# Performance work log

Hardware: AMD Instinct MI355X
Metric: run time of the kernel (lower is better)

The kernel has to match this reference:

```python
import jax, jax.numpy as jnp
import numpy as np

N_NODES = 10000
N_EDGES = 160000
IN_DIM = 512
HID = 256
HEADS = 4
OUT_DIM = 512
NEG_SLOPE = 0.2  # PyG GATConv default


def _glorot(key, shape):
    fan_in, fan_out = shape[0], shape[-1]
    lim = jnp.sqrt(6.0 / (fan_in + fan_out))
    return jax.random.uniform(key, shape, jnp.float32, -lim, lim)


def setup_inputs() -> dict:
    key = jax.random.key(0)
    ks = jax.random.split(key, 16)
    x = jax.random.normal(ks[0], (N_NODES, IN_DIM), jnp.float32)
    edge_index = jax.random.randint(ks[1], (2, N_EDGES), 0, N_NODES, jnp.int64)
    # layer 1: GATConv(512 -> 256, heads=4, concat) -> out 1024
    W1 = _glorot(ks[2], (IN_DIM, HEADS * HID))
    att_src1 = _glorot(ks[3], (HEADS, HID))
    att_dst1 = _glorot(ks[4], (HEADS, HID))
    b1 = jnp.zeros((HEADS * HID,), jnp.float32)
    # layer 2: GATConv(1024 -> 256, heads=4, concat) -> out 1024
    W2 = _glorot(ks[5], (HEADS * HID, HEADS * HID))
    att_src2 = _glorot(ks[6], (HEADS, HID))
    att_dst2 = _glorot(ks[7], (HEADS, HID))
    b2 = jnp.zeros((HEADS * HID,), jnp.float32)
    # final fc: 1024 -> 512
    fcW = _glorot(ks[8], (HEADS * HID, OUT_DIM))
    fcb = jnp.zeros((OUT_DIM,), jnp.float32)
    return dict(x=x, edge_index=edge_index, W1=W1, att_src1=att_src1,
                att_dst1=att_dst1, b1=b1, W2=W2, att_src2=att_src2,
                att_dst2=att_dst2, b2=b2, fcW=fcW, fcb=fcb)


def gat_conv(x, src, dst, W, att_src, att_dst, bias):
    # x: [N, F_in]; src/dst: [E] (self-loops already included)
    N = x.shape[0]
    h = (x @ W).reshape(N, HEADS, HID)                       # [N, H, C]
    a_src = jnp.sum(h * att_src, axis=-1)                    # [N, H]
    a_dst = jnp.sum(h * att_dst, axis=-1)                    # [N, H]
    e = jax.nn.leaky_relu(a_src[src] + a_dst[dst], NEG_SLOPE)  # [E, H]
    # numerically stable segment softmax over destination nodes
    m = jax.ops.segment_max(e, dst, num_segments=N)          # [N, H]
    e = jnp.exp(e - m[dst])
    s = jax.ops.segment_sum(e, dst, num_segments=N)          # [N, H]
    alpha = e / (s[dst] + 1e-16)                             # [E, H]
    msg = alpha[:, :, None] * h[src]                         # [E, H, C]
    out = jax.ops.segment_sum(msg, dst, num_segments=N)      # [N, H, C]
    return out.reshape(N, HEADS * HID) + bias


def reference(x, edge_index, W1, att_src1, att_dst1, b1,
              W2, att_src2, att_dst2, b2, fcW, fcb):
    N = x.shape[0]
    loops = jnp.arange(N, dtype=edge_index.dtype)
    src = jnp.concatenate([edge_index[0], loops])  # PyG add_self_loops=True
    dst = jnp.concatenate([edge_index[1], loops])
    h = gat_conv(x, src, dst, W1, att_src1, att_dst1, b1)
    h = jax.nn.relu(h)  # dropout is identity in eval mode
    h = gat_conv(h, src, dst, W2, att_src2, att_dst2, b2)
    h = jax.nn.relu(h)
    return h @ fcW + fcb
```

## Files before the change

kernel.cpp:

```cpp
#include <hip/hip_runtime.h>
#include <hip/hip_bf16.h>

#define NN 10000
#define NE 160000
#define NET 170000
#define IN_DIM 512
#define D1 1024
#define HEADS 4
#define HID 256
#define OUT_DIM 512
#define NEG_SLOPE 0.2f

typedef __attribute__((ext_vector_type(8))) short bf16x8;
typedef __attribute__((ext_vector_type(4))) float f32x4;

__device__ inline float b2f(unsigned short b) {
    union { unsigned u; float f; } x; x.u = ((unsigned)b) << 16; return x.f;
}
__device__ inline unsigned short f2b(float f) {
    union { float f; unsigned u; } x; x.f = f;
    unsigned u = x.u;
    unsigned r = u + 0x7FFFu + ((u >> 16) & 1u);
    return (unsigned short)(r >> 16);
}
__device__ inline float lrelu(float v) { return v > 0.f ? v : NEG_SLOPE * v; }

__global__ void init_kernel(const int* ei32, int* flag, int* counts, int* cursor) {
    int i = blockIdx.x * blockDim.x + threadIdx.x;
    if (i < NN) { counts[i] = 0; cursor[i] = 0; }
    if (blockIdx.x == 0) {
        __shared__ int nz;
        if (threadIdx.x == 0) nz = 0;
        __syncthreads();
        int acc = 0;
        for (int k = threadIdx.x; k < 500; k += 256) acc |= ei32[2 * k + 1];
        if (acc) atomicOr(&nz, 1);
        __syncthreads();
        if (threadIdx.x == 0) flag[0] = (nz == 0) ? 1 : 0;
    }
}

__device__ inline void load_edge(const void* ei, int f64, int e, int& s, int& d) {
    if (f64) {
        const long long* p = (const long long*)ei;
        s = (int)p[e]; d = (int)p[NE + e];
    } else {
        const int* p = (const int*)ei;
        s = p[e]; d = p[NE + e];
    }
}

__global__ void count_kernel(const void* ei, const int* flag, int* counts) {
    int e = blockIdx.x * blockDim.x + threadIdx.x;
    if (e >= NET) return;
    int s, d;
    if (e < NE) load_edge(ei, *flag, e, s, d);
    else d = e - NE;
    atomicAdd(&counts[d], 1);
}

__global__ __launch_bounds__(256) void scan_kernel(const int* counts, int* indptr) {
    __shared__ int part[256];
    int t = threadIdx.x;
    int base = t * 40;
    int local[40];
    int sum = 0;
#pragma unroll
    for (int k = 0; k < 40; k++) {
        int i = base + k;
        int c = (i < NN) ? counts[i] : 0;
        local[k] = sum;
        sum += c;
    }
    part[t] = sum;
    __syncthreads();
    for (int off = 1; off < 256; off <<= 1) {
        int v = (t >= off) ? part[t - off] : 0;
        __syncthreads();
        part[t] += v;
        __syncthreads();
    }
    int excl = part[t] - sum;
#pragma unroll
    for (int k = 0; k < 40; k++) {
        int i = base + k;
        if (i < NN) indptr[i] = excl + local[k];
    }
    if (t == 255) indptr[NN] = part[255];
}

__global__ void fill_kernel(const void* ei, const int* flag, const int* indptr,
                            int* cursor, int* csr_src) {
    int e = blockIdx.x * blockDim.x + threadIdx.x;
    if (e >= NET) return;
    int s, d;
    if (e < NE) load_edge(ei, *flag, e, s, d);
    else { s = e - NE; d = s; }
    int pos = indptr[d] + atomicAdd(&cursor[d], 1);
    csr_src[pos] = s;
}

__device__ void tpose_tile(const float* __restrict__ in, unsigned short* __restrict__ out,
                           int R, int C, int bx, int by) {
    __shared__ float tile[32][33];
    int tx = threadIdx.x & 31, ty = threadIdx.x >> 5;
    int c = bx * 32 + tx;
#pragma unroll
    for (int r0 = 0; r0 < 32; r0 += 8) {
        int r = by * 32 + ty + r0;
        tile[ty + r0][tx] = in[(size_t)r * C + c];
    }
    __syncthreads();
    int oc = by * 32 + tx;
#pragma unroll
    for (int r0 = 0; r0 < 32; r0 += 8) {
        int orow = bx * 32 + ty + r0;
        out[(size_t)orow * R + oc] = f2b(tile[tx][ty + r0]);
    }
}

#define CVT_NB 5000
#define TP1_NB 512
#define TP2_NB 1024
#define TP3_NB 512
__global__ __launch_bounds__(256) void prep_kernel(
    const float* __restrict__ x, unsigned short* __restrict__ xb,
    const float* __restrict__ W1, unsigned short* __restrict__ W1t,
    const float* __restrict__ W2, unsigned short* __restrict__ W2t,
    const float* __restrict__ fcW, unsigned short* __restrict__ fcWt) {
    int b = blockIdx.x;
    if (b < CVT_NB) {
        int i = b * 256 + threadIdx.x;
        float4 v = reinterpret_cast<const float4*>(x)[i];
        ushort4 o;
        o.x = f2b(v.x); o.y = f2b(v.y); o.z = f2b(v.z); o.w = f2b(v.w);
        reinterpret_cast<ushort4*>(xb)[i] = o;
        return;
    }
    b -= CVT_NB;
    if (b < TP1_NB) { tpose_tile(W1, W1t, IN_DIM, D1, b & 31, b >> 5); return; }
    b -= TP1_NB;
    if (b < TP2_NB) { tpose_tile(W2, W2t, D1, D1, b & 31, b >> 5); return; }
    b -= TP2_NB;
    tpose_tile(fcW, fcWt, D1, OUT_DIM, b & 15, b >> 4);
}

template<int TBM, int TBN>
__global__ __launch_bounds__(256) void gemmT(
    const unsigned short* __restrict__ A, const unsigned short* __restrict__ B,
    const float* __restrict__ bias, float* __restrict__ Cf, unsigned short* __restrict__ Cb,
    int M, int N, int K, int NB) {
    constexpr int FM = TBM / 32;
    constexpr int FN = TBN / 32;
    constexpr int AISS = TBM / 32;
    constexpr int BISS = TBN / 32;
    __shared__ __align__(16) unsigned short As[TBM * 64];
    __shared__ __align__(16) unsigned short Bs[TBN * 64];
    int t = threadIdx.x;
    int nwg = gridDim.x;
    int q = nwg >> 3, r = nwg & 7;
    int xcd = blockIdx.x & 7, jj = blockIdx.x >> 3;
    int wg = (xcd < r ? xcd * (q + 1) : r * (q + 1) + (xcd - r) * q) + jj;
    int row0 = (wg / NB) * TBM, col0 = (wg % NB) * TBN;

    int w = t >> 6, l = t & 63;
    int wr = w >> 1, wc = w & 1;
    f32x4 acc[FM][FN] = {};

    int srow = w * 8 + (l >> 3);
    int scs = ((l & 7) ^ (l >> 3)) * 8;
    const unsigned short* ap[AISS];
    const unsigned short* bp[BISS];
    unsigned short* asd[AISS];
    unsigned short* bsd[BISS];
#pragma unroll
    for (int i = 0; i < AISS; i++) {
        ap[i] = A + (size_t)min(row0 + i * 32 + srow, M - 1) * K + scs;
        asd[i] = As + i * 2048 + w * 512;
    }
#pragma unroll
    for (int i = 0; i < BISS; i++) {
        bp[i] = B + (size_t)(col0 + i * 32 + srow) * K + scs;
        bsd[i] = Bs + i * 2048 + w * 512;
    }

    int rr = l & 15;
    int rb = (rr & 7) << 4;
    int kb0 = (l >> 4) << 4;
    const char* Ab = (const char*)As;
    const char* Bb = (const char*)Bs;

#define GLD(src, dst) __builtin_amdgcn_global_load_lds( \
        (const __attribute__((address_space(1))) void*)(src), \
        (__attribute__((address_space(3))) void*)(dst), 16, 0, 0)

    for (int k0 = 0; k0 < K; k0 += 64) {
#pragma unroll
        for (int i = 0; i < AISS; i++) { GLD(ap[i], asd[i]); ap[i] += 64; }
#pragma unroll
        for (int i = 0; i < BISS; i++) { GLD(bp[i], bsd[i]); bp[i] += 64; }
        __syncthreads();

#pragma unroll
        for (int ks = 0; ks < 2; ks++) {
            int kb = ((ks << 6) | kb0) ^ rb;
            bf16x8 af[FM], bfv[FN];
#pragma unroll
            for (int mi = 0; mi < FM; mi++)
                af[mi] = *reinterpret_cast<const bf16x8*>(
                    Ab + (wr * (TBM / 2) + mi * 16 + rr) * 128 + kb);
#pragma unroll
            for (int ni = 0; ni < FN; ni++)
                bfv[ni] = *reinterpret_cast<const bf16x8*>(
                    Bb + (wc * (TBN / 2) + ni * 16 + rr) * 128 + kb);
#pragma unroll
            for (int mi = 0; mi < FM; mi++)
#pragma unroll
                for (int ni = 0; ni < FN; ni++)
                    acc[mi][ni] = __builtin_amdgcn_mfma_f32_16x16x32_bf16(
                        af[mi], bfv[ni], acc[mi][ni], 0, 0, 0);
        }
        __syncthreads();
    }
#undef GLD

    int c_l = l & 15, r_h = (l >> 4) * 4;
#pragma unroll
    for (int mi = 0; mi < FM; mi++)
#pragma unroll
        for (int ni = 0; ni < FN; ni++) {
            int gc = col0 + wc * (TBN / 2) + ni * 16 + c_l;
#pragma unroll
            for (int j = 0; j < 4; j++) {
                int gr = row0 + wr * (TBM / 2) + mi * 16 + r_h + j;
                if (gr < M) {
                    float v = acc[mi][ni][j];
                    if (bias) v += bias[gc];
                    if (Cf) Cf[(size_t)gr * N + gc] = v;
                    if (Cb) Cb[(size_t)gr * N + gc] = f2b(v);
                }
            }
        }
}

__global__ __launch_bounds__(256) void att_kernel(const unsigned short* __restrict__ hb,
                                                  const float* __restrict__ att_s,
                                                  const float* __restrict__ att_d,
                                                  float* __restrict__ aS, float* __restrict__ aD) {
    int node = blockIdx.x * 4 + (threadIdx.x >> 6);
    int l = threadIdx.x & 63;
    int head = l >> 4, qq = l & 15;
    const unsigned short* hrow = hb + (size_t)node * D1 + head * HID + qq * 16;
    bf16x8 h0 = *reinterpret_cast<const bf16x8*>(hrow);
    bf16x8 h1 = *reinterpret_cast<const bf16x8*>(hrow + 8);
    const float* asp = att_s + head * HID + qq * 16;
    const float* adp = att_d + head * HID + qq * 16;
    float ps = 0.f, pd = 0.f;
#pragma unroll
    for (int c = 0; c < 8; c++) {
        float hv = b2f((unsigned short)h0[c]);
        float hw = b2f((unsigned short)h1[c]);
        ps += hv * asp[c] + hw * asp[8 + c];
        pd += hv * adp[c] + hw * adp[8 + c];
    }
#pragma unroll
    for (int off = 1; off <= 8; off <<= 1) {
        ps += __shfl_xor(ps, off);
        pd += __shfl_xor(pd, off);
    }
    if (qq == 0) {
        aS[node * HEADS + head] = ps;
        aD[node * HEADS + head] = pd;
    }
}

__global__ __launch_bounds__(256) void agg_kernel(const unsigned short* __restrict__ hb,
                                                  const float* __restrict__ aS,
                                                  const float* __restrict__ aD,
                                                  const int* __restrict__ indptr,
                                                  const int* __restrict__ csr_src,
                                                  const float* __restrict__ bias,
                                                  unsigned short* __restrict__ outb) {
    int node = blockIdx.x * 4 + (threadIdx.x >> 6);
    int l = threadIdx.x & 63;
    int head = l >> 4;
    int beg = indptr[node];
    int deg = indptr[node + 1] - beg;
    float adst = aD[node * HEADS + head];
    const unsigned short* hp = hb + (size_t)l * 16;
    const int* cs = csr_src + beg;
    float acc[16];
#pragma unroll
    for (int c = 0; c < 16; c++) acc[c] = 0.f;
    float esum = 0.f;
    int dm = deg - 1;
    for (int j = 0; j < deg; j += 4) {
        int i0 = j, i1 = min(j + 1, dm), i2 = min(j + 2, dm), i3 = min(j + 3, dm);
        int s0 = cs[i0], s1 = cs[i1], s2 = cs[i2], s3 = cs[i3];
        const unsigned short* r0 = hp + (size_t)s0 * D1;
        const unsigned short* r1 = hp + (size_t)s1 * D1;
        const unsigned short* r2 = hp + (size_t)s2 * D1;
        const unsigned short* r3 = hp + (size_t)s3 * D1;
        bf16x8 r0a = *reinterpret_cast<const bf16x8*>(r0);
        bf16x8 r0b = *reinterpret_cast<const bf16x8*>(r0 + 8);
        bf16x8 r1a = *reinterpret_cast<const bf16x8*>(r1);
        bf16x8 r1b = *reinterpret_cast<const bf16x8*>(r1 + 8);
        bf16x8 r2a = *reinterpret_cast<const bf16x8*>(r2);
        bf16x8 r2b = *reinterpret_cast<const bf16x8*>(r2 + 8);
        bf16x8 r3a = *reinterpret_cast<const bf16x8*>(r3);
        bf16x8 r3b = *reinterpret_cast<const bf16x8*>(r3 + 8);
        float e0 = __expf(lrelu(aS[s0 * HEADS + head] + adst));
        float e1 = (j + 1 <= dm) ? __expf(lrelu(aS[s1 * HEADS + head] + adst)) : 0.f;
        float e2 = (j + 2 <= dm) ? __expf(lrelu(aS[s2 * HEADS + head] + adst)) : 0.f;
        float e3 = (j + 3 <= dm) ? __expf(lrelu(aS[s3 * HEADS + head] + adst)) : 0.f;
        esum += e0 + e1 + e2 + e3;
#pragma unroll
        for (int c = 0; c < 8; c++) {
            acc[c] += e0 * b2f((unsigned short)r0a[c]) + e1 * b2f((unsigned short)r1a[c])
                    + e2 * b2f((unsigned short)r2a[c]) + e3 * b2f((unsigned short)r3a[c]);
            acc[8 + c] += e0 * b2f((unsigned short)r0b[c]) + e1 * b2f((unsigned short)r1b[c])
                        + e2 * b2f((unsigned short)r2b[c]) + e3 * b2f((unsigned short)r3b[c]);
        }
    }
    float inv = 1.f / (esum + 1e-16f);
    const float* bp = bias + l * 16;
    bf16x8 o0, o1;
#pragma unroll
    for (int c = 0; c < 8; c++) {
        o0[c] = (short)f2b(fmaxf(acc[c] * inv + bp[c], 0.f));
        o1[c] = (short)f2b(fmaxf(acc[8 + c] * inv + bp[8 + c], 0.f));
    }
    unsigned short* op = outb + (size_t)node * D1 + l * 16;
    *reinterpret_cast<bf16x8*>(op) = o0;
    *reinterpret_cast<bf16x8*>(op + 8) = o1;
}

extern "C" void kernel_launch(void* const* d_in, const int* in_sizes, int n_in,
                              void* d_out, int out_size, void* d_ws, size_t ws_size,
                              hipStream_t stream) {
    const float* x   = (const float*)d_in[0];
    const void*  ei  = d_in[1];
    const float* W1  = (const float*)d_in[2];
    const float* as1 = (const float*)d_in[3];
    const float* ad1 = (const float*)d_in[4];
    const float* b1  = (const float*)d_in[5];
    const float* W2  = (const float*)d_in[6];
    const float* as2 = (const float*)d_in[7];
    const float* ad2 = (const float*)d_in[8];
    const float* b2  = (const float*)d_in[9];
    const float* fcW = (const float*)d_in[10];
    const float* fcb = (const float*)d_in[11];
    float* out = (float*)d_out;

    char* ws = (char*)d_ws;
    size_t o = 0;
    auto carve = [&](size_t bytes) -> char* {
        char* p = ws + o;
        o = (o + bytes + 255) & ~(size_t)255;
        return p;
    };
    unsigned short* xb   = (unsigned short*)carve((size_t)NN * IN_DIM * 2);
    unsigned short* hb   = (unsigned short*)carve((size_t)NN * D1 * 2);
    unsigned short* x2b  = (unsigned short*)carve((size_t)NN * D1 * 2);
    unsigned short* W1t  = (unsigned short*)carve((size_t)D1 * IN_DIM * 2);
    unsigned short* W2t  = (unsigned short*)carve((size_t)D1 * D1 * 2);
    unsigned short* fcWt = (unsigned short*)carve((size_t)OUT_DIM * D1 * 2);
    float* aS   = (float*)carve((size_t)NN * HEADS * 4);
    float* aD   = (float*)carve((size_t)NN * HEADS * 4);
    int* counts = (int*)carve((size_t)NN * 4);
    int* cursor = (int*)carve((size_t)NN * 4);
    int* indptr = (int*)carve((size_t)(NN + 1) * 4);
    int* csr_src= (int*)carve((size_t)NET * 4);
    int* flag   = (int*)carve(4);
    (void)ws_size; (void)in_sizes; (void)n_in; (void)out_size;

    init_kernel<<<(NN + 255) / 256, 256, 0, stream>>>((const int*)ei, flag, counts, cursor);
    count_kernel<<<(NET + 255) / 256, 256, 0, stream>>>(ei, flag, counts);
    scan_kernel<<<1, 256, 0, stream>>>(counts, indptr);
    fill_kernel<<<(NET + 255) / 256, 256, 0, stream>>>(ei, flag, indptr, cursor, csr_src);

    prep_kernel<<<CVT_NB + TP1_NB + TP2_NB + TP3_NB, 256, 0, stream>>>(
        x, xb, W1, W1t, W2, W2t, fcW, fcWt);

    const int MB128 = (NN + 127) / 128;
    const int MB64  = (NN + 63) / 64;
    gemmT<128, 64><<<MB128 * (D1 / 64), 256, 0, stream>>>(xb, W1t, nullptr, nullptr, hb,
                                                          NN, D1, IN_DIM, D1 / 64);
    att_kernel<<<NN / 4, 256, 0, stream>>>(hb, as1, ad1, aS, aD);
    agg_kernel<<<NN / 4, 256, 0, stream>>>(hb, aS, aD, indptr, csr_src, b1, x2b);
    gemmT<128, 64><<<MB128 * (D1 / 64), 256, 0, stream>>>(x2b, W2t, nullptr, nullptr, hb,
                                                          NN, D1, D1, D1 / 64);
    att_kernel<<<NN / 4, 256, 0, stream>>>(hb, as2, ad2, aS, aD);
    agg_kernel<<<NN / 4, 256, 0, stream>>>(hb, aS, aD, indptr, csr_src, b2, x2b);
    gemmT<64, 64><<<MB64 * (OUT_DIM / 64), 256, 0, stream>>>(x2b, fcWt, fcb, out, nullptr,
                                                             NN, OUT_DIM, D1, OUT_DIM / 64);
}
```

Measured before the change: 240.9 us.

## Double-buffer GEMM LDS tiles and merge init into setup kernel

The bf16 MFMA GEMM now keeps two LDS buffers and issues the global-to-LDS loads for the next K tile before computing the current one. This leaves one barrier per iteration instead of two and lets load latency overlap with MFMA work. The separate init kernel is also folded into the prep kernel as extra blocks, which saves one launch. Doubling LDS per workgroup may lower occupancy, and the overlap relies on the single barrier correctly ordering buffer reuse.

```diff
diff --git a/kernel.cpp b/kernel.cpp
--- a/kernel.cpp
+++ b/kernel.cpp
@@ -25,21 +25,6 @@
 }
 __device__ inline float lrelu(float v) { return v > 0.f ? v : NEG_SLOPE * v; }
 
-__global__ void init_kernel(const int* ei32, int* flag, int* counts, int* cursor) {
-    int i = blockIdx.x * blockDim.x + threadIdx.x;
-    if (i < NN) { counts[i] = 0; cursor[i] = 0; }
-    if (blockIdx.x == 0) {
-        __shared__ int nz;
-        if (threadIdx.x == 0) nz = 0;
-        __syncthreads();
-        int acc = 0;
-        for (int k = threadIdx.x; k < 500; k += 256) acc |= ei32[2 * k + 1];
-        if (acc) atomicOr(&nz, 1);
-        __syncthreads();
-        if (threadIdx.x == 0) flag[0] = (nz == 0) ? 1 : 0;
-    }
-}
-
 __device__ inline void load_edge(const void* ei, int f64, int e, int& s, int& d) {
     if (f64) {
         const long long* p = (const long long*)ei;
@@ -119,16 +104,34 @@
     }
 }
 
+#define INIT_NB 40
 #define CVT_NB 5000
 #define TP1_NB 512
 #define TP2_NB 1024
 #define TP3_NB 512
-__global__ __launch_bounds__(256) void prep_kernel(
+__global__ __launch_bounds__(256) void setup_kernel(
+    const int* ei32, int* flag, int* counts, int* cursor,
     const float* __restrict__ x, unsigned short* __restrict__ xb,
     const float* __restrict__ W1, unsigned short* __restrict__ W1t,
     const float* __restrict__ W2, unsigned short* __restrict__ W2t,
     const float* __restrict__ fcW, unsigned short* __restrict__ fcWt) {
     int b = blockIdx.x;
+    if (b < INIT_NB) {
+        int i = b * 256 + threadIdx.x;
+        if (i < NN) { counts[i] = 0; cursor[i] = 0; }
+        if (b == 0) {
+            __shared__ int nz;
+            if (threadIdx.x == 0) nz = 0;
+            __syncthreads();
+            int acc = 0;
+            for (int k = threadIdx.x; k < 500; k += 256) acc |= ei32[2 * k + 1];
+            if (acc) atomicOr(&nz, 1);
+            __syncthreads();
+            if (threadIdx.x == 0) flag[0] = (nz == 0) ? 1 : 0;
+        }
+        return;
+    }
+    b -= INIT_NB;
     if (b < CVT_NB) {
         int i = b * 256 + threadIdx.x;
         float4 v = reinterpret_cast<const float4*>(x)[i];
@@ -154,8 +157,10 @@
     constexpr int FN = TBN / 32;
     constexpr int AISS = TBM / 32;
     constexpr int BISS = TBN / 32;
-    __shared__ __align__(16) unsigned short As[TBM * 64];
-    __shared__ __align__(16) unsigned short Bs[TBN * 64];
+    constexpr int ABUF = TBM * 64;
+    constexpr int BBUF = TBN * 64;
+    __shared__ __align__(16) unsigned short As[2 * ABUF];
+    __shared__ __align__(16) unsigned short Bs[2 * BBUF];
     int t = threadIdx.x;
     int nwg = gridDim.x;
     int q = nwg >> 3, r = nwg & 7;
@@ -171,36 +176,45 @@
     int scs = ((l & 7) ^ (l >> 3)) * 8;
     const unsigned short* ap[AISS];
     const unsigned short* bp[BISS];
-    unsigned short* asd[AISS];
-    unsigned short* bsd[BISS];
-#pragma unroll
-    for (int i = 0; i < AISS; i++) {
+#pragma unroll
+    for (int i = 0; i < AISS; i++)
         ap[i] = A + (size_t)min(row0 + i * 32 + srow, M - 1) * K + scs;
-        asd[i] = As + i * 2048 + w * 512;
-    }
-#pragma unroll
-    for (int i = 0; i < BISS; i++) {
+#pragma unroll
+    for (int i = 0; i < BISS; i++)
         bp[i] = B + (size_t)(col0 + i * 32 + srow) * K + scs;
-        bsd[i] = Bs + i * 2048 + w * 512;
-    }
 
     int rr = l & 15;
     int rb = (rr & 7) << 4;
     int kb0 = (l >> 4) << 4;
-    const char* Ab = (const char*)As;
-    const char* Bb = (const char*)Bs;
+    int c_l = l & 15, r_h = (l >> 4) * 4;
 
 #define GLD(src, dst) __builtin_amdgcn_global_load_lds( \
         (const __attribute__((address_space(1))) void*)(src), \
         (__attribute__((address_space(3))) void*)(dst), 16, 0, 0)
 
+#pragma unroll
+    for (int i = 0; i < AISS; i++) { GLD(ap[i], As + i * 2048 + w * 512); ap[i] += 64; }
+#pragma unroll
+    for (int i = 0; i < BISS; i++) { GLD(bp[i], Bs + i * 2048 + w * 512); bp[i] += 64; }
+    __syncthreads();
+
+    int cur = 0;
     for (int k0 = 0; k0 < K; k0 += 64) {
-#pragma unroll
-        for (int i = 0; i < AISS; i++) { GLD(ap[i], asd[i]); ap[i] += 64; }
-#pragma unroll
-        for (int i = 0; i < BISS; i++) { GLD(bp[i], bsd[i]); bp[i] += 64; }
-        __syncthreads();
-
+        int nxt = cur ^ 1;
+        if (k0 + 64 < K) {
+#pragma unroll
+            for (int i = 0; i < AISS; i++) {
+                GLD(ap[i], As + nxt * ABUF + i * 2048 + w * 512);
+                ap[i] += 64;
+            }
+#pragma unroll
+            for (int i = 0; i < BISS; i++) {
+                GLD(bp[i], Bs + nxt * BBUF + i * 2048 + w * 512);
+                bp[i] += 64;
+            }
+        }
+        const char* Ab = (const char*)(As + cur * ABUF);
+        const char* Bb = (const char*)(Bs + cur * BBUF);
 #pragma unroll
         for (int ks = 0; ks < 2; ks++) {
             int kb = ((ks << 6) | kb0) ^ rb;
@@ -221,10 +235,10 @@
                         af[mi], bfv[ni], acc[mi][ni], 0, 0, 0);
         }
         __syncthreads();
+        cur = nxt;
     }
 #undef GLD
 
-    int c_l = l & 15, r_h = (l >> 4) * 4;
 #pragma unroll
     for (int mi = 0; mi < FM; mi++)
 #pragma unroll
@@ -374,13 +388,11 @@
     int* flag   = (int*)carve(4);
     (void)ws_size; (void)in_sizes; (void)n_in; (void)out_size;
 
-    init_kernel<<<(NN + 255) / 256, 256, 0, stream>>>((const int*)ei, flag, counts, cursor);
+    setup_kernel<<<INIT_NB + CVT_NB + TP1_NB + TP2_NB + TP3_NB, 256, 0, stream>>>(
+        (const int*)ei, flag, counts, cursor, x, xb, W1, W1t, W2, W2t, fcW, fcWt);
     count_kernel<<<(NET + 255) / 256, 256, 0, stream>>>(ei, flag, counts);
     scan_kernel<<<1, 256, 0, stream>>>(counts, indptr);
     fill_kernel<<<(NET + 255) / 256, 256, 0, stream>>>(ei, flag, indptr, cursor, csr_src);
-
-    prep_kernel<<<CVT_NB + TP1_NB + TP2_NB + TP3_NB, 256, 0, stream>>>(
-        x, xb, W1, W1t, W2, W2t, fcW, fcWt);
 
     const int MB128 = (NN + 127) / 128;
     const int MB64  = (NN + 63) / 64;
```

Result: no change. 239.9 us (-0.4%).
